# Optimization experiments

Measured on AMD Instinct MI355X. Metric: run time of the kernel, lower is better.

## Reference

```python
import jax, jax.numpy as jnp
import numpy as np

ETA = 0.1      # self.eta
BETA = 0.05    # self.beta
MU = 0.05      # self.mu
MINI = 1e-6    # mini_val
SEEDS_PER_TOPIC = 10


def setup_inputs() -> dict:
    key = jax.random.key(0)
    k1, k2, k3, k4 = jax.random.split(key, 4)
    B, V, K = 64, 10000, 64
    # sparse-ish bag-of-words counts in {0,1,2}
    batch_BOW = jax.random.randint(k1, (B, V), 0, 3).astype(jnp.float32)
    # disjoint seed words: SEEDS_PER_TOPIC seed words per topic
    seeds = jnp.zeros((V, K), jnp.float32)
    rows = jnp.arange(SEEDS_PER_TOPIC * K)
    cols = jnp.repeat(jnp.arange(K), SEEDS_PER_TOPIC)
    seeds = seeds.at[rows, cols].set(1.0)
    exp_m = jax.random.uniform(k2, (B, K), jnp.float32) * 10.0     # E[m_dk] for docs in batch
    exp_s = jax.random.uniform(k3, (V, K), jnp.float32) * 5.0 * seeds  # E[s_wk], nonzero only at seed entries
    exp_n = jax.random.uniform(k4, (V, K), jnp.float32) * 5.0      # E[n_wk]
    pi = jnp.full((K,), 0.7, jnp.float32)
    return {"batch_BOW": batch_BOW, "seeds": seeds, "exp_m": exp_m,
            "exp_s": exp_s, "exp_n": exp_n, "pi": pi}


def reference(batch_BOW, seeds, exp_m, exp_s, exp_n, pi):
    # Vectorized SCVB0_guided over the whole minibatch (no per-doc Python loop).
    V, K = seeds.shape
    S = seeds.sum(0)                      # [K] number of seed words per topic
    beta_sum = BETA * V                   # self.beta_sum[guided_m]
    mu_sum = MU * S                       # [K]
    exp_s_sum = exp_s.sum(0)              # [K]
    exp_n_sum = exp_n.sum(0)              # [K]

    mask = (batch_BOW > 0).astype(batch_BOW.dtype)[:, :, None]   # [B,V,1] BOW_nonzero gather
    theta = exp_m[:, None, :] + ETA                               # [B,1,K]
    phi_s = (MU + exp_s) / (mu_sum + exp_s_sum)                   # [V,K]
    phi_n = (BETA + exp_n) / (beta_sum + exp_n_sum)               # [V,K]

    g_ss = mask * seeds[None] * theta * phi_s[None] * pi          # [B,V,K]
    g_sr = mask * seeds[None] * theta * phi_n[None] * (1.0 - pi)
    g_rr = mask * (1.0 - seeds[None]) * theta * phi_n[None]

    s_sum = g_ss.sum(-1, keepdims=True) + g_sr.sum(-1, keepdims=True)
    r_sum = g_rr.sum(-1, keepdims=True)
    g_ss = g_ss / (s_sum + MINI)
    g_sr = g_sr / (s_sum + MINI)
    g_rr = g_rr / (r_sum + MINI)

    # seed word <=> word is seed of at least one topic; else use g_rr only
    is_seed = (seeds.sum(1) > 0)[None, :, None]                   # [1,V,1]
    gamma = jnp.where(is_seed, pi * g_ss + (1.0 - pi) * (g_sr + g_rr), g_rr)

    counts = batch_BOW[:, :, None]                                # [B,V,1]
    temp_exp_m_batch = (gamma * counts).sum(1)                    # [B,K]
    temp_exp_n = ((g_sr + g_rr) * counts).sum(0)                  # [V,K] scatter-accumulate
    temp_exp_s = (g_ss * counts).sum(0)                           # [V,K]
    gamma_sr_sum = g_sr.sum((0, 1))                               # [K]
    exp_q_z = (gamma * jnp.log(gamma + MINI)).sum()               # scalar entropy term
    return temp_exp_m_batch, temp_exp_n, temp_exp_s, gamma_sr_sum, exp_q_z
```

## Files before the change

kernel.cpp:

```cpp
#include <hip/hip_runtime.h>
#include <hip/hip_bf16.h>

#define ETA_C  0.1f
#define BETA_C 0.05f
#define MU_C   0.05f
#define MINI_C 1e-6f

typedef __attribute__((ext_vector_type(8))) short short8;
typedef __attribute__((ext_vector_type(4))) float f32x4;

template<int CTRL, int ROWMASK>
__device__ __forceinline__ float dpp_add(float x) {
  int v = __builtin_amdgcn_update_dpp(0, __float_as_int(x), CTRL, ROWMASK, 0xf, true);
  return x + __int_as_float(v);
}

__device__ __forceinline__ float wave_sum(float x) {
  x = dpp_add<0xB1,  0xF>(x);
  x = dpp_add<0x4E,  0xF>(x);
  x = dpp_add<0x141, 0xF>(x);
  x = dpp_add<0x140, 0xF>(x);
  x = dpp_add<0x142, 0xA>(x);
  x = dpp_add<0x143, 0xC>(x);
  return __int_as_float(__builtin_amdgcn_readlane(__float_as_int(x), 63));
}

__device__ __forceinline__ float rl(float x, int k) {
  return __int_as_float(__builtin_amdgcn_readlane(__float_as_int(x), k));
}

__device__ __forceinline__ short bf16r(float x) {
  unsigned u = __float_as_uint(x);
  u += 0x7fffu + ((u >> 16) & 1u);
  return (short)(u >> 16);
}

__device__ __forceinline__ float bf2f(short s) {
  return __uint_as_float(((unsigned)(unsigned short)s) << 16);
}

__global__ __launch_bounds__(256) void sums_kernel(
    const float* __restrict__ seeds, const float* __restrict__ es,
    const float* __restrict__ en, float* __restrict__ part,
    float* __restrict__ out, int V, int rows_per_block, int gsr_off) {
  __shared__ float sh[192];
  int t = threadIdx.x, bx = blockIdx.x;
  if (bx < 16) out[(bx << 8) + t] = 0.f;
  else if (bx == 16 && t < 65) out[gsr_off + t] = 0.f;
  if (t < 192) sh[t] = 0.f;
  __syncthreads();
  int k = t & 63, w = t >> 6;
  int v0 = bx * rows_per_block;
  int v1 = min(v0 + rows_per_block, V);
  float s0 = 0.f, s1 = 0.f, s2 = 0.f;
  for (int v = v0 + w; v < v1; v += 4) {
    int idx = (v << 6) + k;
    s0 += seeds[idx]; s1 += es[idx]; s2 += en[idx];
  }
  atomicAdd(&sh[k], s0);
  atomicAdd(&sh[64 + k], s1);
  atomicAdd(&sh[128 + k], s2);
  __syncthreads();
  if (t < 192) part[bx * 192 + t] = sh[t];
}

__global__ __launch_bounds__(1024, 4) void main_kernel(
    const float* __restrict__ bow,
    const float* __restrict__ seeds,
    const float* __restrict__ exp_m,
    const float* __restrict__ exp_s,
    const float* __restrict__ exp_n,
    const float* __restrict__ pi,
    const float* __restrict__ part,
    float* __restrict__ out,
    int V, int gsr_off, int NB) {
  __shared__ short THbf[4096];
  __shared__ short THTbf[4096];
  __shared__ short TLbf[4096];
  __shared__ short ARRT[1024];
  __shared__ short ASVT[1024];
  __shared__ short ARLT[1024];
  __shared__ short WSRT[2048];
  __shared__ short PKA[2048];
  __shared__ short CIRT[1024];
  __shared__ float RSL[64 * 17];
  __shared__ float SSL[64 * 17];
  __shared__ float L0a[64 * 17];
  __shared__ float L0b[64 * 17];
  __shared__ float sums_sh[192];
  float* NNL = RSL;
  float* red_gsr = SSL;
  float* redq = L0a;

  int t = threadIdx.x;
#pragma unroll
  for (int i = 0; i < 4; i++) {
    int idx = t + (i << 10);
    int b = idx >> 6, k = idx & 63;
    float th = exp_m[idx] + ETA_C;
    float lth = __logf(th);
    THbf[idx] = bf16r(th);
    THTbf[(k << 6) + b] = bf16r(th);
    TLbf[idx] = bf16r(th * lth);
  }
  if (t < 192) {
    float s = 0.f;
#pragma unroll 8
    for (int j = 0; j < 64; j++) s += part[j * 192 + t];
    sums_sh[t] = s;
  }
  __syncthreads();

  int lane = t & 63, w = t >> 6;
  int q = lane >> 4, c = lane & 15;
  float acc_g_tot = 0.f, acc_q_tot = 0.f;
  f32x4 accP = {0.f, 0.f, 0.f, 0.f};

  for (int tile = blockIdx.x; tile < NB; tile += gridDim.x) {
    int v = (tile << 4) + w;
    bool active = (v < V);

    float pik = 0.f, omp = 0.f, a_ss = 0.f, a_sr = 0.f, a_rr = 0.f;
    float bowpre = 0.f;
    bool seedRow = false;
    if (active) {
      int rbase = (v << 6) + lane;
      float seed = seeds[rbase];
      float es = exp_s[rbase];
      float en = exp_n[rbase];
      pik = pi[lane];
      float inv_ds = __builtin_amdgcn_rcpf(MU_C * sums_sh[lane] + sums_sh[64 + lane]);
      float inv_dn = __builtin_amdgcn_rcpf(BETA_C * (float)V + sums_sh[128 + lane]);
      float phi_s = (MU_C + es) * inv_ds;
      float phi_n = (BETA_C + en) * inv_dn;
      omp = 1.0f - pik;
      a_ss = seed * phi_s * pik;
      a_sr = seed * phi_n * omp;
      a_rr = (1.0f - seed) * phi_n;
      seedRow = (__ballot(seed > 0.f) != 0ull);
      float wsv = fmaf(pik, a_ss, omp * a_sr);
      float wrv = seedRow ? omp * a_rr : a_rr;
      float arrl = (a_rr > 0.f) ? a_rr * __logf(a_rr) : 0.f;
      ARRT[(w << 6) + lane] = bf16r(a_rr);
      ASVT[(w << 6) + lane] = bf16r(a_ss + a_sr);
      ARLT[(w << 6) + lane] = bf16r(arrl);
      WSRT[(lane << 5) + w] = bf16r(wsv);
      WSRT[(lane << 5) + 16 + w] = bf16r(wrv);
      bowpre = bow[lane * V + v];
    } else {
      ARRT[(w << 6) + lane] = 0;
      ASVT[(w << 6) + lane] = 0;
      ARLT[(w << 6) + lane] = 0;
      WSRT[(lane << 5) + w] = 0;
      WSRT[(lane << 5) + 16 + w] = 0;
    }
    __syncthreads();

    {
      int job = w >> 2, mt = w & 3;
      const short* Amat = (job == 3) ? TLbf : THbf;
      const short* Bmat = (job == 0) ? ARRT : (job == 1) ? ASVT
                         : (job == 2) ? ARLT : ARRT;
      float* Cd = (job == 0) ? RSL : (job == 1) ? SSL : (job == 2) ? L0a : L0b;
      f32x4 acc = {0.f, 0.f, 0.f, 0.f};
      int arow = (mt << 4) + c;
#pragma unroll
      for (int s = 0; s < 2; s++) {
        short8 af = *(const short8*)&Amat[(arow << 6) + (s << 5) + (q << 3)];
        short8 bf = *(const short8*)&Bmat[(c << 6) + (s << 5) + (q << 3)];
        acc = __builtin_amdgcn_mfma_f32_16x16x32_bf16(af, bf, acc, 0, 0, 0);
      }
#pragma unroll
      for (int r = 0; r < 4; r++)
        Cd[((mt << 4) + (q << 2) + r) * 17 + c] = acc[r];
    }
    __syncthreads();

    float acc_s = 0.f, acc_g = 0.f, acc_qk = 0.f, acc_qb = 0.f;
    if (active) {
      float rsv = RSL[lane * 17 + w];
      float ssv = SSL[lane * 17 + w];
      float ivx = __builtin_amdgcn_rcpf(ssv + MINI_C);
      float ivy = __builtin_amdgcn_rcpf(rsv + MINI_C);
      float cis = bowpre * ivx;
      float cirr = bowpre * ivy;
      PKA[(lane << 5) + w] = bf16r(cis);
      PKA[(lane << 5) + 16 + w] = bf16r(cirr);
      CIRT[(w << 6) + lane] = bf16r(cirr);
      if (!seedRow) {
        float Lb = L0a[lane * 17 + w] + L0b[lane * 17 + w];
        float q0 = (bowpre > 0.f) ? ivy : 0.f;
        float q1 = q0 * __logf(ivy);
        acc_qb = fmaf(q0, Lb, q1 * rsv);
        out[4096 + V * 64 + (v << 6) + lane] = 0.f;
      } else {
        float acc_n = 0.f;
        unsigned long long m = __ballot(bowpre > 0.f);
        while (m) {
          int b = __builtin_amdgcn_readfirstlane(__builtin_ctzll(m));
          m &= (m - 1);
          float cb = rl(bowpre, b);
          float is = rl(ivx, b), ir = rl(ivy, b);
          float th = bf2f(THbf[(b << 6) + lane]);
          float gss = th * a_ss * is;
          float gsr = th * a_sr * is;
          float grr = th * a_rr * ir;
          float gnr = gsr + grr;
          float gamma = fmaf(pik, gss, omp * gnr);
          acc_n = fmaf(gnr, cb, acc_n);
          acc_s = fmaf(gss, cb, acc_s);
          acc_g += gsr;
          acc_qk = fmaf(gamma, __logf(gamma + MINI_C), acc_qk);
        }
        out[4096 + (v << 6) + lane] = acc_n;
        out[4096 + V * 64 + (v << 6) + lane] = acc_s;
      }
    } else {
      PKA[(lane << 5) + w] = 0;
      PKA[(lane << 5) + 16 + w] = 0;
      CIRT[(w << 6) + lane] = 0;
    }
    acc_g_tot += acc_g;
    acc_q_tot += acc_qk + acc_qb;
    __syncthreads();

    {
      int tm = w >> 2, tn = w & 3;
      short8 af = *(const short8*)&PKA[(((tm << 4) + c) << 5) + (q << 3)];
      short8 bf = *(const short8*)&WSRT[(((tn << 4) + c) << 5) + (q << 3)];
      accP = __builtin_amdgcn_mfma_f32_16x16x32_bf16(af, bf, accP, 0, 0, 0);
      if (w >= 12) {
        int mt = w - 12;
        f32x4 an = {0.f, 0.f, 0.f, 0.f};
#pragma unroll
        for (int s = 0; s < 2; s++) {
          short8 a2 = *(const short8*)&THTbf[(((mt << 4) + c) << 6) + (s << 5) + (q << 3)];
          short8 b2 = *(const short8*)&CIRT[(c << 6) + (s << 5) + (q << 3)];
          an = __builtin_amdgcn_mfma_f32_16x16x32_bf16(a2, b2, an, 0, 0, 0);
        }
#pragma unroll
        for (int r = 0; r < 4; r++)
          NNL[((mt << 4) + (q << 2) + r) * 17 + c] = an[r];
      }
    }
    __syncthreads();

    if (active && !seedRow)
      out[4096 + (v << 6) + lane] = a_rr * NNL[lane * 17 + w];
  }

  {
    int tm = w >> 2, tn = w & 3;
#pragma unroll
    for (int r = 0; r < 4; r++) {
      int brow = (tm << 4) + (q << 2) + r;
      int kcol = (tn << 4) + c;
      float val = accP[r] * bf2f(THbf[(brow << 6) + kcol]);
      atomicAdd(&out[(brow << 6) + kcol], val);
    }
  }
  __syncthreads();
  red_gsr[t] = acc_g_tot;
  float qzw = wave_sum(acc_q_tot);
  if (lane == 0) redq[w] = qzw;
  __syncthreads();

  if (w == 0) {
    float g = 0.f;
#pragma unroll
    for (int j = 0; j < 16; j++) g += red_gsr[(j << 6) + lane];
    if (g != 0.f) atomicAdd(&out[gsr_off + lane], g);
    if (t == 0) {
      float qs = 0.f;
#pragma unroll
      for (int j = 0; j < 16; j++) qs += redq[j];
      atomicAdd(&out[gsr_off + 64], qs);
    }
  }
}

extern "C" void kernel_launch(void* const* d_in, const int* in_sizes, int n_in,
                              void* d_out, int out_size, void* d_ws,
                              size_t ws_size, hipStream_t stream) {
  (void)n_in; (void)out_size; (void)ws_size;
  const float* bow   = (const float*)d_in[0];
  const float* seeds = (const float*)d_in[1];
  const float* exp_m = (const float*)d_in[2];
  const float* exp_s = (const float*)d_in[3];
  const float* exp_n = (const float*)d_in[4];
  const float* pi    = (const float*)d_in[5];
  int K = in_sizes[5];
  int V = in_sizes[1] / K;
  float* out = (float*)d_out;
  float* part = (float*)d_ws;

  int NB = (V + 15) / 16;
  int NP = NB < 512 ? NB : 512;
  int gsr_off = 4096 + 2 * V * 64;
  int rpb = (V + 63) / 64;

  sums_kernel<<<64, 256, 0, stream>>>(seeds, exp_s, exp_n, part, out, V, rpb,
                                      gsr_off);
  main_kernel<<<NP, 1024, 0, stream>>>(bow, seeds, exp_m, exp_s, exp_n, pi,
                                       part, out, V, gsr_off, NB);
}
```

Baseline: 111.7 us.

## Prefetch next tile's inputs, parallelize partial-sum reduction, move zero-fill to sums kernel

The main loop now software-prefetches the seeds, exp_s, exp_n and bow values for the next tile into registers while the current tile is computed, hiding global load latency. The reduction of the 64 per-block partial sums is split across 960 threads in five chunks and combined through shared memory. Zeroing of the temp_exp_s output region moves from the per-row non-seed path into a vectorized float4 fill in the sums kernel. Costs are extra register pressure from the prefetched values and an extra barrier, and any seed row that does not write all of its entries now depends on that early zero-fill.

```diff
diff --git a/kernel.cpp b/kernel.cpp
--- a/kernel.cpp
+++ b/kernel.cpp
@@ -47,6 +47,12 @@
   int t = threadIdx.x, bx = blockIdx.x;
   if (bx < 16) out[(bx << 8) + t] = 0.f;
   else if (bx == 16 && t < 65) out[gsr_off + t] = 0.f;
+  {
+    float4* dst = (float4*)(out + 4096 + (size_t)V * 64);
+    int n4 = (V * 64) >> 2;
+    for (int i = bx * 256 + t; i < n4; i += 64 * 256)
+      dst[i] = make_float4(0.f, 0.f, 0.f, 0.f);
+  }
   if (t < 192) sh[t] = 0.f;
   __syncthreads();
   int k = t & 63, w = t >> 6;
@@ -73,7 +79,7 @@
     const float* __restrict__ pi,
     const float* __restrict__ part,
     float* __restrict__ out,
-    int V, int gsr_off, int NB) {
+    int V, int gsr_off, int NB, int NP) {
   __shared__ short THbf[4096];
   __shared__ short THTbf[4096];
   __shared__ short TLbf[4096];
@@ -91,6 +97,7 @@
   float* NNL = RSL;
   float* red_gsr = SSL;
   float* redq = L0a;
+  float* part5 = RSL;
 
   int t = threadIdx.x;
 #pragma unroll
@@ -103,12 +110,18 @@
     THTbf[(k << 6) + b] = bf16r(th);
     TLbf[idx] = bf16r(th * lth);
   }
-  if (t < 192) {
+  if (t < 960) {
+    int c = t % 192, chunk = t / 192;
+    int r0 = chunk * 13;
+    int r1 = min(r0 + 13, 64);
     float s = 0.f;
-#pragma unroll 8
-    for (int j = 0; j < 64; j++) s += part[j * 192 + t];
-    sums_sh[t] = s;
-  }
+    for (int r = r0; r < r1; r++) s += part[r * 192 + c];
+    part5[chunk * 192 + c] = s;
+  }
+  __syncthreads();
+  if (t < 192)
+    sums_sh[t] = ((part5[t] + part5[192 + t]) + (part5[384 + t] + part5[576 + t]))
+                 + part5[768 + t];
   __syncthreads();
 
   int lane = t & 63, w = t >> 6;
@@ -116,18 +129,36 @@
   float acc_g_tot = 0.f, acc_q_tot = 0.f;
   f32x4 accP = {0.f, 0.f, 0.f, 0.f};
 
-  for (int tile = blockIdx.x; tile < NB; tile += gridDim.x) {
+  float p_seed = 0.f, p_es = 0.f, p_en = 0.f, p_bow = 0.f;
+  {
+    int vv = (blockIdx.x << 4) + w;
+    if (vv < V) {
+      int rb = (vv << 6) + lane;
+      p_seed = seeds[rb]; p_es = exp_s[rb]; p_en = exp_n[rb];
+      p_bow = bow[lane * V + vv];
+    }
+  }
+
+  for (int tile = blockIdx.x; tile < NB; tile += NP) {
     int v = (tile << 4) + w;
     bool active = (v < V);
+    float seed = p_seed, es = p_es, en = p_en, bowpre = p_bow;
+
+    {
+      int nt = tile + NP;
+      int vv = (nt << 4) + w;
+      if (vv < V) {
+        int rb = (vv << 6) + lane;
+        p_seed = seeds[rb]; p_es = exp_s[rb]; p_en = exp_n[rb];
+        p_bow = bow[lane * V + vv];
+      } else {
+        p_seed = p_es = p_en = p_bow = 0.f;
+      }
+    }
 
     float pik = 0.f, omp = 0.f, a_ss = 0.f, a_sr = 0.f, a_rr = 0.f;
-    float bowpre = 0.f;
     bool seedRow = false;
     if (active) {
-      int rbase = (v << 6) + lane;
-      float seed = seeds[rbase];
-      float es = exp_s[rbase];
-      float en = exp_n[rbase];
       pik = pi[lane];
       float inv_ds = __builtin_amdgcn_rcpf(MU_C * sums_sh[lane] + sums_sh[64 + lane]);
       float inv_dn = __builtin_amdgcn_rcpf(BETA_C * (float)V + sums_sh[128 + lane]);
@@ -146,7 +177,6 @@
       ARLT[(w << 6) + lane] = bf16r(arrl);
       WSRT[(lane << 5) + w] = bf16r(wsv);
       WSRT[(lane << 5) + 16 + w] = bf16r(wrv);
-      bowpre = bow[lane * V + v];
     } else {
       ARRT[(w << 6) + lane] = 0;
       ASVT[(w << 6) + lane] = 0;
@@ -192,7 +222,6 @@
         float q0 = (bowpre > 0.f) ? ivy : 0.f;
         float q1 = q0 * __logf(ivy);
         acc_qb = fmaf(q0, Lb, q1 * rsv);
-        out[4096 + V * 64 + (v << 6) + lane] = 0.f;
       } else {
         float acc_n = 0.f;
         unsigned long long m = __ballot(bowpre > 0.f);
@@ -302,5 +331,5 @@
   sums_kernel<<<64, 256, 0, stream>>>(seeds, exp_s, exp_n, part, out, V, rpb,
                                       gsr_off);
   main_kernel<<<NP, 1024, 0, stream>>>(bow, seeds, exp_m, exp_s, exp_n, pi,
-                                       part, out, V, gsr_off, NB);
-}
+                                       part, out, V, gsr_off, NB, NP);
+}
```

Result: slower. 114.3 us (+2.3%).
